# Performance work log

Hardware: AMD Instinct MI355X
Metric: run time of the kernel (lower is better)

## Reference

```python
import jax, jax.numpy as jnp
import numpy as np

N, IN, OUT, K = 4096, 512, 256, 3
ALPHA, BETA, ETA = 0.2, 0.1, 0.5
NEG_INF = -9e15


def setup_inputs() -> dict:
    key = jax.random.key(0)
    k1, k2, k3, k4, k5, k6 = jax.random.split(key, 6)
    h = jax.random.normal(k1, (N, IN), dtype=jnp.float32)
    # xavier-ish scale for params
    W = jax.random.normal(k2, (K * IN, OUT), dtype=jnp.float32) * (1.414 / np.sqrt(IN + OUT))
    a = jax.random.normal(k3, (2 * OUT * K, 1), dtype=jnp.float32) * 0.05
    disc = jax.random.normal(k4, (2 * OUT, 1), dtype=jnp.float32) * 0.05
    k_mask = jax.random.randint(k5, (K, N, N), 0, 2).astype(jnp.int32)  # 0/1 k-hop masks
    lamda = jax.random.uniform(k6, (1,), dtype=jnp.float32)
    return {"h": h, "W": W, "a": a, "disc": disc, "k_mask": k_mask, "lamda": lamda}


def reference(h, W, a, disc, k_mask, lamda):
    lam = lamda[0]
    Wk = W.reshape(K, IN, OUT)          # W[i*IN:(i+1)*IN] per hop
    ak = a.reshape(K, 2, OUT)           # a[2*hop*OUT:(2*hop+2)*OUT] per hop, split in two
    d = disc.reshape(2, OUT)

    # Per-hop projections. In the torch loop Wh is recomputed from h each hop,
    # so only hop 0 determines the returned features; all hops feed dischange.
    Wh_all = jnp.einsum('ni,kio->kno', h, Wk)  # [K, N, OUT]

    # dischange = sum_i eta^i * (Wh_i @ d1 + (Wh_i @ d2).T)  -- rank-1 separable
    wts = ETA ** jnp.arange(K, dtype=jnp.float32)            # [K]
    dv1 = jnp.einsum('kno,o->kn', Wh_all, d[0])              # [K, N]
    dv2 = jnp.einsum('kno,o->kn', Wh_all, d[1])
    u = jnp.einsum('k,kn->n', wts, dv1)
    v = jnp.einsum('k,kn->n', wts, dv2)
    dischange = u[:, None] + v[None, :]                      # [N, N]

    # hop-0 masked GAT attention
    Wh0 = Wh_all[0]
    s1 = Wh0 @ ak[0, 0]                                      # [N]
    s2 = Wh0 @ ak[0, 1]
    e = jax.nn.leaky_relu(s1[:, None] + s2[None, :], ALPHA)  # [N, N]
    att = jax.nn.softmax(jnp.where(k_mask[0] > 0, e, NEG_INF), axis=1)
    # dropout disabled (eval mode / training=False)
    Wh = (1.0 - BETA) * (att @ Wh0) + BETA * Wh0
    out = jax.nn.elu(Wh)

    # normalize dischange and threshold against lamda
    dn = dischange / jnp.maximum(jnp.abs(dischange.min()), dischange.max())
    pos = (dn > lam).astype(jnp.int32)
    dn = jnp.where(dn > lam, 0.0, dn)
    neg = (dn < -lam).astype(jnp.int32)
    dn = jnp.where(dn < -lam, 0.0, dn)

    # mask lists computed from ORIGINAL masks, then applied sequentially
    pos_list = [((k_mask[i] + pos) >= 2).astype(jnp.int32) for i in range(K - 1)]
    neg_list = [((k_mask[i] + neg) >= 2).astype(jnp.int32) for i in range(1, K)]
    km = k_mask
    for i in range(1, K):
        km = km.at[i].add(pos_list[i - 1])
        km = km.at[i - 1].add(-pos_list[i - 1])
    for i in range(K - 1):
        km = km.at[i + 1].add(neg_list[i])
        km = km.at[i].add(-neg_list[i])

    return out, dn, km
```

## Files before the change

### kernel.cpp

```cpp
#include <hip/hip_runtime.h>
#include <hip/hip_bf16.h>
#include <math.h>

#define N 4096
#define DIN 512
#define DOUT 256
#define JS 8
#define JCH (N / JS)

typedef short bf16x8 __attribute__((ext_vector_type(8)));
typedef float f32x4 __attribute__((ext_vector_type(4)));
typedef int i32x4 __attribute__((ext_vector_type(4)));

static __device__ __forceinline__ unsigned short f2bf(float x) {
  __hip_bfloat16 b = __float2bfloat16(x);
  return __builtin_bit_cast(unsigned short, b);
}

static __device__ __forceinline__ unsigned int f2ord(float f) {
  unsigned int b = __float_as_uint(f);
  return (b & 0x80000000u) ? ~b : (b | 0x80000000u);
}
static __device__ __forceinline__ float ord2f(unsigned int u) {
  unsigned int b = (u & 0x80000000u) ? (u ^ 0x80000000u) : ~u;
  return __uint_as_float(b);
}

__global__ __launch_bounds__(256) void k_pq(const float* __restrict__ W,
                                            const float* __restrict__ disc,
                                            double* __restrict__ p, double* __restrict__ q,
                                            unsigned int* __restrict__ smaxw) {
  if (blockIdx.x == 0 && threadIdx.x == 0) smaxw[0] = 0u;
  __shared__ double lds[8];
  int i = blockIdx.x;
  int t = threadIdx.x;
  double accp = 0.0, accq = 0.0;
  const double wts[3] = {1.0, 0.5, 0.25};
#pragma unroll
  for (int k = 0; k < 3; ++k) {
    double w = (double)W[((size_t)(k * DIN + i)) * DOUT + t];
    accp += wts[k] * w * (double)disc[t];
    accq += wts[k] * w * (double)disc[DOUT + t];
  }
  for (int off = 32; off; off >>= 1) { accp += __shfl_down(accp, off); accq += __shfl_down(accq, off); }
  int l = t & 63, w_ = t >> 6;
  if (l == 0) { lds[w_] = accp; lds[4 + w_] = accq; }
  __syncthreads();
  if (t == 0) {
    p[i] = lds[0] + lds[1] + lds[2] + lds[3];
    q[i] = lds[4] + lds[5] + lds[6] + lds[7];
  }
}

__global__ __launch_bounds__(256) void k_uv(const float* __restrict__ h,
                                            const double* __restrict__ p, const double* __restrict__ q,
                                            double* __restrict__ u, double* __restrict__ v) {
  __shared__ double lds[8];
  int n = blockIdx.x, t = threadIdx.x;
  double su = 0.0, sv = 0.0;
#pragma unroll
  for (int i = t; i < DIN; i += 256) {
    double hv = (double)h[(size_t)n * DIN + i];
    su += hv * p[i];
    sv += hv * q[i];
  }
  for (int off = 32; off; off >>= 1) { su += __shfl_down(su, off); sv += __shfl_down(sv, off); }
  int l = t & 63, w_ = t >> 6;
  if (l == 0) { lds[w_] = su; lds[4 + w_] = sv; }
  __syncthreads();
  if (t == 0) {
    u[n] = lds[0] + lds[1] + lds[2] + lds[3];
    v[n] = lds[4] + lds[5] + lds[6] + lds[7];
  }
}

__global__ __launch_bounds__(1024) void k_denom(const double* __restrict__ u,
                                                const double* __restrict__ v,
                                                double* __restrict__ scal) {
  __shared__ double lds[64];
  int t = threadIdx.x;
  double mnu = 1e300, mxu = -1e300, mnv = 1e300, mxv = -1e300;
#pragma unroll
  for (int k = 0; k < 4; ++k) {
    double uu = u[t + k * 1024], vv = v[t + k * 1024];
    mnu = fmin(mnu, uu); mxu = fmax(mxu, uu);
    mnv = fmin(mnv, vv); mxv = fmax(mxv, vv);
  }
  for (int off = 32; off; off >>= 1) {
    mnu = fmin(mnu, __shfl_down(mnu, off)); mxu = fmax(mxu, __shfl_down(mxu, off));
    mnv = fmin(mnv, __shfl_down(mnv, off)); mxv = fmax(mxv, __shfl_down(mxv, off));
  }
  int l = t & 63, w_ = t >> 6;
  if (l == 0) { lds[w_] = mnu; lds[16 + w_] = mxu; lds[32 + w_] = mnv; lds[48 + w_] = mxv; }
  __syncthreads();
  if (t == 0) {
    double a = 1e300, b = -1e300, c = 1e300, d = -1e300;
    for (int k = 0; k < 16; ++k) {
      a = fmin(a, lds[k]); b = fmax(b, lds[16 + k]);
      c = fmin(c, lds[32 + k]); d = fmax(d, lds[48 + k]);
    }
    double mn = a + c, mx = b + d;
    scal[0] = 1.0 / fmax(fabs(mn), mx);
  }
}

__global__ __launch_bounds__(256) void k_dnkm(const int* __restrict__ kmask,
                                              const double* __restrict__ u, const double* __restrict__ v,
                                              const double* __restrict__ scal, const float* __restrict__ lamda,
                                              float* __restrict__ dn, float* __restrict__ kmout) {
  const size_t NN = (size_t)N * N;
  const int* k0 = kmask; const int* k1 = kmask + NN; const int* k2 = kmask + 2 * NN;
  float* km0 = kmout; float* km1 = kmout + NN; float* km2 = kmout + 2 * NN;
  const size_t total4 = NN / 4;
  double inv = scal[0];
  double lam = (double)lamda[0];
  for (size_t idx = (size_t)blockIdx.x * 256 + threadIdx.x; idx < total4;
       idx += (size_t)gridDim.x * 256) {
    int i = (int)(idx >> 10);
    int j = (int)(idx & 1023) << 2;
    size_t base = (size_t)i * N + j;
    double ui = u[i];
    double2 va = *(const double2*)(v + j);
    double2 vb = *(const double2*)(v + j + 2);
    double vv[4] = {va.x, va.y, vb.x, vb.y};
    i32x4 m0 = __builtin_nontemporal_load((const i32x4*)(k0 + base));
    i32x4 m1 = __builtin_nontemporal_load((const i32x4*)(k1 + base));
    i32x4 m2 = __builtin_nontemporal_load((const i32x4*)(k2 + base));
    f32x4 odn, o0, o1, o2;
#pragma unroll
    for (int c = 0; c < 4; ++c) {
      double dnv = (ui + vv[c]) * inv;
      bool pos = dnv > lam, neg = dnv < -lam;
      float dnf = (pos || neg) ? 0.0f : (float)dnv;
      int mk0 = m0[c], mk1 = m1[c], mk2 = m2[c];
      int p0 = pos ? mk0 : 0;
      int p1 = pos ? mk1 : 0;
      int n0 = neg ? mk1 : 0;
      int n1 = neg ? mk2 : 0;
      odn[c] = dnf;
      o0[c] = (float)(mk0 - p0 - n0);
      o1[c] = (float)(mk1 + p0 - p1 + n0 - n1);
      o2[c] = (float)(mk2 + p1 + n1);
    }
    __builtin_nontemporal_store(odn, (f32x4*)(dn + base));
    __builtin_nontemporal_store(o0, (f32x4*)(km0 + base));
    __builtin_nontemporal_store(o1, (f32x4*)(km1 + base));
    __builtin_nontemporal_store(o2, (f32x4*)(km2 + base));
  }
}

__global__ __launch_bounds__(256) void k_wh0(const float* __restrict__ h, const float* __restrict__ W,
                                             float* __restrict__ Wh0, unsigned short* __restrict__ Wh0T) {
  __shared__ float As[32][20];
  __shared__ float Bs[16][72];
  int t = threadIdx.x;
  int i0 = blockIdx.x * 32, o0 = blockIdx.y * 64;
  int tx = t & 15, ty = t >> 4;
  float acc[2][4] = {};
  int am = t >> 2, ak = (t & 3) * 4;
  int bk = t >> 4, bn = (t & 15) * 4;
  float4 pa, pb;
  if (t < 128) pa = *(const float4*)(h + (size_t)(i0 + am) * DIN + ak);
  pb = *(const float4*)(W + (size_t)bk * DOUT + o0 + bn);
  for (int kb = 0; kb < DIN; kb += 16) {
    if (t < 128) *(float4*)&As[am][ak] = pa;
    *(float4*)&Bs[bk][bn] = pb;
    __syncthreads();
    if (kb + 16 < DIN) {
      if (t < 128) pa = *(const float4*)(h + (size_t)(i0 + am) * DIN + kb + 16 + ak);
      pb = *(const float4*)(W + (size_t)(kb + 16 + bk) * DOUT + o0 + bn);
    }
#pragma unroll
    for (int kk = 0; kk < 16; ++kk) {
      float a0 = As[ty * 2 + 0][kk], a1 = As[ty * 2 + 1][kk];
      float4 b = *(const float4*)&Bs[kk][tx * 4];
      acc[0][0] += a0 * b.x; acc[0][1] += a0 * b.y; acc[0][2] += a0 * b.z; acc[0][3] += a0 * b.w;
      acc[1][0] += a1 * b.x; acc[1][1] += a1 * b.y; acc[1][2] += a1 * b.z; acc[1][3] += a1 * b.w;
    }
    __syncthreads();
  }
#pragma unroll
  for (int r = 0; r < 2; ++r) {
    int n = i0 + ty * 2 + r;
    float4 vo = {acc[r][0], acc[r][1], acc[r][2], acc[r][3]};
    *(float4*)(Wh0 + (size_t)n * DOUT + o0 + tx * 4) = vo;
#pragma unroll
    for (int c = 0; c < 4; ++c) {
      Wh0T[(size_t)(o0 + tx * 4 + c) * N + n] = f2bf(acc[r][c]);
    }
  }
}

__global__ __launch_bounds__(256) void k_s1s2(const float* __restrict__ Wh0, const float* __restrict__ a,
                                              float* __restrict__ s1, float* __restrict__ s2,
                                              unsigned int* __restrict__ smaxw) {
  __shared__ float lds[8];
  int i = blockIdx.x, t = threadIdx.x;
  float val = Wh0[(size_t)i * DOUT + t];
  float v1 = val * a[t];
  float v2 = val * a[DOUT + t];
  for (int off = 32; off; off >>= 1) { v1 += __shfl_down(v1, off); v2 += __shfl_down(v2, off); }
  int l = t & 63, w_ = t >> 6;
  if (l == 0) { lds[w_] = v1; lds[4 + w_] = v2; }
  __syncthreads();
  if (t == 0) {
    s1[i] = lds[0] + lds[1] + lds[2] + lds[3];
    float s2i = lds[4] + lds[5] + lds[6] + lds[7];
    s2[i] = s2i;
    atomicMax(smaxw, f2ord(s2i));
  }
}

__global__ __launch_bounds__(512) void k_attn2(const int* __restrict__ k0,
                                               const float* __restrict__ s1, const float* __restrict__ s2,
                                               const unsigned int* __restrict__ smaxw,
                                               const unsigned short* __restrict__ Wh0T,
                                               float* __restrict__ Opart, float* __restrict__ Zpart) {
  int t = threadIdx.x;
  int w = t >> 6, l = t & 63;
  int o0 = (w & 3) * 64;
  int rbase = blockIdx.x * 32 + (w >> 2) * 16;
  int row = l & 15;
  int kg = l >> 4;
  int irow = rbase + row;
  float s1r = s1[irow];
  float sm2 = ord2f(smaxw[0]);
  float mb = s1r + sm2;
  float mi = mb >= 0.0f ? mb : 0.2f * mb;
  f32x4 acc0 = {0,0,0,0}, acc1 = {0,0,0,0}, acc2 = {0,0,0,0}, acc3 = {0,0,0,0};
  float zacc = 0.0f;
  const unsigned short* bbase = Wh0T + ((size_t)(o0 + row) * N + 8 * kg);
  const int* mbase = k0 + (size_t)irow * N + 8 * kg;
  const float* sbase = s2 + 8 * kg;
  int jbeg = blockIdx.y * JCH;
  for (int j0 = jbeg; j0 < jbeg + JCH; j0 += 32) {
    int4 ma = *(const int4*)(mbase + j0);
    int4 mb4 = *(const int4*)(mbase + j0 + 4);
    float4 sa = *(const float4*)(sbase + j0);
    float4 sb = *(const float4*)(sbase + j0 + 4);
    float pv[8];
#pragma unroll
    for (int c = 0; c < 4; ++c) {
      float sv = s1r + (&sa.x)[c];
      float e = sv >= 0.0f ? sv : 0.2f * sv;
      pv[c] = (&ma.x)[c] > 0 ? __expf(e - mi) : 0.0f;
    }
#pragma unroll
    for (int c = 0; c < 4; ++c) {
      float sv = s1r + (&sb.x)[c];
      float e = sv >= 0.0f ? sv : 0.2f * sv;
      pv[4 + c] = (&mb4.x)[c] > 0 ? __expf(e - mi) : 0.0f;
    }
    bf16x8 af;
#pragma unroll
    for (int c = 0; c < 8; ++c) af[c] = (short)f2bf(pv[c]);
    zacc += pv[0] + pv[1] + pv[2] + pv[3] + pv[4] + pv[5] + pv[6] + pv[7];
    bf16x8 b0 = *(const bf16x8*)(bbase + j0);
    bf16x8 b1 = *(const bf16x8*)(bbase + 16 * N + j0);
    bf16x8 b2 = *(const bf16x8*)(bbase + 32 * N + j0);
    bf16x8 b3 = *(const bf16x8*)(bbase + 48 * N + j0);
    acc0 = __builtin_amdgcn_mfma_f32_16x16x32_bf16(af, b0, acc0, 0, 0, 0);
    acc1 = __builtin_amdgcn_mfma_f32_16x16x32_bf16(af, b1, acc1, 0, 0, 0);
    acc2 = __builtin_amdgcn_mfma_f32_16x16x32_bf16(af, b2, acc2, 0, 0, 0);
    acc3 = __builtin_amdgcn_mfma_f32_16x16x32_bf16(af, b3, acc3, 0, 0, 0);
  }
  zacc += __shfl_xor(zacc, 16);
  zacc += __shfl_xor(zacc, 32);
  if ((w & 3) == 0 && l < 16) Zpart[(size_t)blockIdx.y * N + rbase + l] = zacc;
  float* op = Opart + (size_t)blockIdx.y * N * DOUT;
  int col = l & 15, rw = (l >> 4) * 4;
  f32x4 accs[4] = {acc0, acc1, acc2, acc3};
#pragma unroll
  for (int reg = 0; reg < 4; ++reg) {
    int i = rbase + rw + reg;
#pragma unroll
    for (int os = 0; os < 4; ++os) {
      op[(size_t)i * DOUT + o0 + os * 16 + col] = accs[os][reg];
    }
  }
}

__global__ __launch_bounds__(256) void k_ored(const float* __restrict__ Opart,
                                              const float* __restrict__ Zpart,
                                              const float* __restrict__ Wh0,
                                              float* __restrict__ out) {
  int i = blockIdx.x, t = threadIdx.x;
  size_t idx = (size_t)i * DOUT + t;
  float s = 0.0f, z = 0.0f;
#pragma unroll
  for (int sp = 0; sp < JS; ++sp) {
    s += Opart[(size_t)sp * N * DOUT + idx];
    z += Zpart[(size_t)sp * N + i];
  }
  float val = 0.9f * (s / z) + 0.1f * Wh0[idx];
  out[idx] = val > 0.0f ? val : expm1f(val);
}

extern "C" void kernel_launch(void* const* d_in, const int* in_sizes, int n_in,
                              void* d_out, int out_size, void* d_ws, size_t ws_size,
                              hipStream_t stream) {
  const float* h     = (const float*)d_in[0];
  const float* W     = (const float*)d_in[1];
  const float* a     = (const float*)d_in[2];
  const float* disc  = (const float*)d_in[3];
  const int*   kmask = (const int*)d_in[4];
  const float* lamda = (const float*)d_in[5];

  float* out = (float*)d_out;
  float* dn  = out + (size_t)N * DOUT;
  float* km  = dn + (size_t)N * N;

  char* ws = (char*)d_ws;
  double* p    = (double*)ws;
  double* q    = (double*)(ws + 4096);
  double* u    = (double*)(ws + 8192);
  double* v    = (double*)(ws + 8192 + 32768);
  double* scal = (double*)(ws + 8192 + 65536);
  char* ws2 = ws + 8192 + 65536 + 256;
  float* s1            = (float*)ws2;
  float* s2            = (float*)(ws2 + 16384);
  unsigned int* smaxw  = (unsigned int*)(ws2 + 32768);
  float* Zpart         = (float*)(ws2 + 33024);
  char* ws3 = ws2 + 33024 + (size_t)JS * N * 4;
  float* Wh0           = (float*)ws3;
  unsigned short* Wh0T = (unsigned short*)(ws3 + (size_t)N * DOUT * 4);
  float* Opart         = (float*)(ws3 + (size_t)N * DOUT * 6);

  k_pq<<<DIN, 256, 0, stream>>>(W, disc, p, q, smaxw);
  k_uv<<<N, 256, 0, stream>>>(h, p, q, u, v);
  k_denom<<<1, 1024, 0, stream>>>(u, v, scal);
  k_dnkm<<<4096, 256, 0, stream>>>(kmask, u, v, scal, lamda, dn, km);
  k_wh0<<<dim3(N / 32, DOUT / 64), 256, 0, stream>>>(h, W, Wh0, Wh0T);
  k_s1s2<<<N, 256, 0, stream>>>(Wh0, a, s1, s2, smaxw);
  k_attn2<<<dim3(N / 32, JS), 512, 0, stream>>>(kmask, s1, s2, smaxw, Wh0T, Opart, Zpart);
  k_ored<<<N, 256, 0, stream>>>(Opart, Zpart, Wh0, out);
}
```

Before: 603.5 us.

## Fuse attention-probability computation into k-mask streaming pass and s1/s2 into GEMM

The masked softmax numerators are now computed inside the pass that already streams k_mask[0] for the dn/km outputs. They are written as a bf16 probability matrix P along with per-row sums Z, so the attention MFMA kernel no longer rereads the int32 mask or recomputes exp. The s1/s2 dot products are folded into the Wh0 GEMM epilogue via atomics, and the max reduction moves into a combined prep kernel. This removes a second full read of the 64 MB mask, at the cost of writing and reading a 32 MB bf16 P matrix.

After: 539.6 us. -10.6%, faster.

```diff
diff --git a/kernel.cpp b/kernel.cpp
--- a/kernel.cpp
+++ b/kernel.cpp
@@ -11,29 +11,22 @@
 typedef short bf16x8 __attribute__((ext_vector_type(8)));
 typedef float f32x4 __attribute__((ext_vector_type(4)));
 typedef int i32x4 __attribute__((ext_vector_type(4)));
+typedef unsigned short u16x4 __attribute__((ext_vector_type(4)));
 
 static __device__ __forceinline__ unsigned short f2bf(float x) {
   __hip_bfloat16 b = __float2bfloat16(x);
   return __builtin_bit_cast(unsigned short, b);
 }
 
-static __device__ __forceinline__ unsigned int f2ord(float f) {
-  unsigned int b = __float_as_uint(f);
-  return (b & 0x80000000u) ? ~b : (b | 0x80000000u);
-}
-static __device__ __forceinline__ float ord2f(unsigned int u) {
-  unsigned int b = (u & 0x80000000u) ? (u ^ 0x80000000u) : ~u;
-  return __uint_as_float(b);
-}
-
 __global__ __launch_bounds__(256) void k_pq(const float* __restrict__ W,
                                             const float* __restrict__ disc,
                                             double* __restrict__ p, double* __restrict__ q,
-                                            unsigned int* __restrict__ smaxw) {
-  if (blockIdx.x == 0 && threadIdx.x == 0) smaxw[0] = 0u;
-  __shared__ double lds[8];
+                                            float* __restrict__ s1, float* __restrict__ s2) {
   int i = blockIdx.x;
   int t = threadIdx.x;
+  if (i < 16) s1[i * 256 + t] = 0.0f;
+  else if (i < 32) s2[(i - 16) * 256 + t] = 0.0f;
+  __shared__ double lds[8];
   double accp = 0.0, accq = 0.0;
   const double wts[3] = {1.0, 0.5, 0.25};
 #pragma unroll
@@ -74,83 +67,10 @@
   }
 }
 
-__global__ __launch_bounds__(1024) void k_denom(const double* __restrict__ u,
-                                                const double* __restrict__ v,
-                                                double* __restrict__ scal) {
-  __shared__ double lds[64];
-  int t = threadIdx.x;
-  double mnu = 1e300, mxu = -1e300, mnv = 1e300, mxv = -1e300;
-#pragma unroll
-  for (int k = 0; k < 4; ++k) {
-    double uu = u[t + k * 1024], vv = v[t + k * 1024];
-    mnu = fmin(mnu, uu); mxu = fmax(mxu, uu);
-    mnv = fmin(mnv, vv); mxv = fmax(mxv, vv);
-  }
-  for (int off = 32; off; off >>= 1) {
-    mnu = fmin(mnu, __shfl_down(mnu, off)); mxu = fmax(mxu, __shfl_down(mxu, off));
-    mnv = fmin(mnv, __shfl_down(mnv, off)); mxv = fmax(mxv, __shfl_down(mxv, off));
-  }
-  int l = t & 63, w_ = t >> 6;
-  if (l == 0) { lds[w_] = mnu; lds[16 + w_] = mxu; lds[32 + w_] = mnv; lds[48 + w_] = mxv; }
-  __syncthreads();
-  if (t == 0) {
-    double a = 1e300, b = -1e300, c = 1e300, d = -1e300;
-    for (int k = 0; k < 16; ++k) {
-      a = fmin(a, lds[k]); b = fmax(b, lds[16 + k]);
-      c = fmin(c, lds[32 + k]); d = fmax(d, lds[48 + k]);
-    }
-    double mn = a + c, mx = b + d;
-    scal[0] = 1.0 / fmax(fabs(mn), mx);
-  }
-}
-
-__global__ __launch_bounds__(256) void k_dnkm(const int* __restrict__ kmask,
-                                              const double* __restrict__ u, const double* __restrict__ v,
-                                              const double* __restrict__ scal, const float* __restrict__ lamda,
-                                              float* __restrict__ dn, float* __restrict__ kmout) {
-  const size_t NN = (size_t)N * N;
-  const int* k0 = kmask; const int* k1 = kmask + NN; const int* k2 = kmask + 2 * NN;
-  float* km0 = kmout; float* km1 = kmout + NN; float* km2 = kmout + 2 * NN;
-  const size_t total4 = NN / 4;
-  double inv = scal[0];
-  double lam = (double)lamda[0];
-  for (size_t idx = (size_t)blockIdx.x * 256 + threadIdx.x; idx < total4;
-       idx += (size_t)gridDim.x * 256) {
-    int i = (int)(idx >> 10);
-    int j = (int)(idx & 1023) << 2;
-    size_t base = (size_t)i * N + j;
-    double ui = u[i];
-    double2 va = *(const double2*)(v + j);
-    double2 vb = *(const double2*)(v + j + 2);
-    double vv[4] = {va.x, va.y, vb.x, vb.y};
-    i32x4 m0 = __builtin_nontemporal_load((const i32x4*)(k0 + base));
-    i32x4 m1 = __builtin_nontemporal_load((const i32x4*)(k1 + base));
-    i32x4 m2 = __builtin_nontemporal_load((const i32x4*)(k2 + base));
-    f32x4 odn, o0, o1, o2;
-#pragma unroll
-    for (int c = 0; c < 4; ++c) {
-      double dnv = (ui + vv[c]) * inv;
-      bool pos = dnv > lam, neg = dnv < -lam;
-      float dnf = (pos || neg) ? 0.0f : (float)dnv;
-      int mk0 = m0[c], mk1 = m1[c], mk2 = m2[c];
-      int p0 = pos ? mk0 : 0;
-      int p1 = pos ? mk1 : 0;
-      int n0 = neg ? mk1 : 0;
-      int n1 = neg ? mk2 : 0;
-      odn[c] = dnf;
-      o0[c] = (float)(mk0 - p0 - n0);
-      o1[c] = (float)(mk1 + p0 - p1 + n0 - n1);
-      o2[c] = (float)(mk2 + p1 + n1);
-    }
-    __builtin_nontemporal_store(odn, (f32x4*)(dn + base));
-    __builtin_nontemporal_store(o0, (f32x4*)(km0 + base));
-    __builtin_nontemporal_store(o1, (f32x4*)(km1 + base));
-    __builtin_nontemporal_store(o2, (f32x4*)(km2 + base));
-  }
-}
-
 __global__ __launch_bounds__(256) void k_wh0(const float* __restrict__ h, const float* __restrict__ W,
-                                             float* __restrict__ Wh0, unsigned short* __restrict__ Wh0T) {
+                                             const float* __restrict__ a,
+                                             float* __restrict__ Wh0, unsigned short* __restrict__ Wh0T,
+                                             float* __restrict__ s1, float* __restrict__ s2) {
   __shared__ float As[32][20];
   __shared__ float Bs[16][72];
   int t = threadIdx.x;
@@ -179,6 +99,8 @@
     }
     __syncthreads();
   }
+  float4 a1v = *(const float4*)(a + o0 + tx * 4);
+  float4 a2v = *(const float4*)(a + DOUT + o0 + tx * 4);
 #pragma unroll
   for (int r = 0; r < 2; ++r) {
     int n = i0 + ty * 2 + r;
@@ -188,34 +110,119 @@
     for (int c = 0; c < 4; ++c) {
       Wh0T[(size_t)(o0 + tx * 4 + c) * N + n] = f2bf(acc[r][c]);
     }
-  }
-}
-
-__global__ __launch_bounds__(256) void k_s1s2(const float* __restrict__ Wh0, const float* __restrict__ a,
-                                              float* __restrict__ s1, float* __restrict__ s2,
-                                              unsigned int* __restrict__ smaxw) {
-  __shared__ float lds[8];
-  int i = blockIdx.x, t = threadIdx.x;
-  float val = Wh0[(size_t)i * DOUT + t];
-  float v1 = val * a[t];
-  float v2 = val * a[DOUT + t];
-  for (int off = 32; off; off >>= 1) { v1 += __shfl_down(v1, off); v2 += __shfl_down(v2, off); }
+    float p1 = acc[r][0] * a1v.x + acc[r][1] * a1v.y + acc[r][2] * a1v.z + acc[r][3] * a1v.w;
+    float p2 = acc[r][0] * a2v.x + acc[r][1] * a2v.y + acc[r][2] * a2v.z + acc[r][3] * a2v.w;
+    for (int off = 1; off < 16; off <<= 1) { p1 += __shfl_xor(p1, off); p2 += __shfl_xor(p2, off); }
+    if (tx == 0) { atomicAdd(s1 + n, p1); atomicAdd(s2 + n, p2); }
+  }
+}
+
+__global__ __launch_bounds__(1024) void k_prep(const double* __restrict__ u,
+                                               const double* __restrict__ v,
+                                               const float* __restrict__ s2,
+                                               double* __restrict__ scal,
+                                               float* __restrict__ smaxf) {
+  __shared__ double lds[64];
+  __shared__ float lf[16];
+  int t = threadIdx.x;
+  double mnu = 1e300, mxu = -1e300, mnv = 1e300, mxv = -1e300;
+#pragma unroll
+  for (int k = 0; k < 4; ++k) {
+    double uu = u[t + k * 1024], vv = v[t + k * 1024];
+    mnu = fmin(mnu, uu); mxu = fmax(mxu, uu);
+    mnv = fmin(mnv, vv); mxv = fmax(mxv, vv);
+  }
+  float4 sv = *(const float4*)(s2 + t * 4);
+  float sm = fmaxf(fmaxf(sv.x, sv.y), fmaxf(sv.z, sv.w));
+  for (int off = 32; off; off >>= 1) {
+    mnu = fmin(mnu, __shfl_down(mnu, off)); mxu = fmax(mxu, __shfl_down(mxu, off));
+    mnv = fmin(mnv, __shfl_down(mnv, off)); mxv = fmax(mxv, __shfl_down(mxv, off));
+    sm = fmaxf(sm, __shfl_down(sm, off));
+  }
   int l = t & 63, w_ = t >> 6;
-  if (l == 0) { lds[w_] = v1; lds[4 + w_] = v2; }
+  if (l == 0) { lds[w_] = mnu; lds[16 + w_] = mxu; lds[32 + w_] = mnv; lds[48 + w_] = mxv; lf[w_] = sm; }
   __syncthreads();
   if (t == 0) {
-    s1[i] = lds[0] + lds[1] + lds[2] + lds[3];
-    float s2i = lds[4] + lds[5] + lds[6] + lds[7];
-    s2[i] = s2i;
-    atomicMax(smaxw, f2ord(s2i));
-  }
-}
-
-__global__ __launch_bounds__(512) void k_attn2(const int* __restrict__ k0,
-                                               const float* __restrict__ s1, const float* __restrict__ s2,
-                                               const unsigned int* __restrict__ smaxw,
+    double a = 1e300, b = -1e300, c = 1e300, d = -1e300;
+    float s = -1e30f;
+    for (int k = 0; k < 16; ++k) {
+      a = fmin(a, lds[k]); b = fmax(b, lds[16 + k]);
+      c = fmin(c, lds[32 + k]); d = fmax(d, lds[48 + k]);
+      s = fmaxf(s, lf[k]);
+    }
+    scal[0] = 1.0 / fmax(fabs(a + c), b + d);
+    smaxf[0] = s;
+  }
+}
+
+__global__ __launch_bounds__(256) void k_dnkm(const int* __restrict__ kmask,
+                                              const double* __restrict__ u, const double* __restrict__ v,
+                                              const double* __restrict__ scal, const float* __restrict__ lamda,
+                                              const float* __restrict__ s1, const float* __restrict__ s2,
+                                              const float* __restrict__ smaxf,
+                                              float* __restrict__ dn, float* __restrict__ kmout,
+                                              unsigned short* __restrict__ P, float* __restrict__ Z) {
+  const size_t NN = (size_t)N * N;
+  const int* k0 = kmask; const int* k1 = kmask + NN; const int* k2 = kmask + 2 * NN;
+  float* km0 = kmout; float* km1 = kmout + NN; float* km2 = kmout + 2 * NN;
+  int r = blockIdx.x, t = threadIdx.x;
+  double inv = scal[0];
+  double lam = (double)lamda[0];
+  double ui = u[r];
+  float s1r = s1[r];
+  float mb = s1r + smaxf[0];
+  float mi = mb >= 0.0f ? mb : 0.2f * mb;
+  float zacc = 0.0f;
+#pragma unroll
+  for (int k = 0; k < 4; ++k) {
+    int j = k * 1024 + t * 4;
+    size_t base = (size_t)r * N + j;
+    double2 va = *(const double2*)(v + j);
+    double2 vb = *(const double2*)(v + j + 2);
+    double vv[4] = {va.x, va.y, vb.x, vb.y};
+    i32x4 m0 = __builtin_nontemporal_load((const i32x4*)(k0 + base));
+    i32x4 m1 = __builtin_nontemporal_load((const i32x4*)(k1 + base));
+    i32x4 m2 = __builtin_nontemporal_load((const i32x4*)(k2 + base));
+    float4 sv = *(const float4*)(s2 + j);
+    f32x4 odn, o0, o1, o2;
+    u16x4 pw;
+#pragma unroll
+    for (int c = 0; c < 4; ++c) {
+      double dnv = (ui + vv[c]) * inv;
+      bool pos = dnv > lam, neg = dnv < -lam;
+      float dnf = (pos || neg) ? 0.0f : (float)dnv;
+      int mk0 = m0[c], mk1 = m1[c], mk2 = m2[c];
+      int p0 = pos ? mk0 : 0;
+      int p1 = pos ? mk1 : 0;
+      int n0 = neg ? mk1 : 0;
+      int n1 = neg ? mk2 : 0;
+      odn[c] = dnf;
+      o0[c] = (float)(mk0 - p0 - n0);
+      o1[c] = (float)(mk1 + p0 - p1 + n0 - n1);
+      o2[c] = (float)(mk2 + p1 + n1);
+      float e = s1r + (&sv.x)[c];
+      e = e >= 0.0f ? e : 0.2f * e;
+      float pv = mk0 > 0 ? __expf(e - mi) : 0.0f;
+      pw[c] = f2bf(pv);
+      zacc += pv;
+    }
+    __builtin_nontemporal_store(odn, (f32x4*)(dn + base));
+    __builtin_nontemporal_store(o0, (f32x4*)(km0 + base));
+    __builtin_nontemporal_store(o1, (f32x4*)(km1 + base));
+    __builtin_nontemporal_store(o2, (f32x4*)(km2 + base));
+    *(u16x4*)(P + base) = pw;
+  }
+  __shared__ float lf[4];
+  for (int off = 32; off; off >>= 1) zacc += __shfl_down(zacc, off);
+  int l = t & 63, w_ = t >> 6;
+  if (l == 0) lf[w_] = zacc;
+  __syncthreads();
+  if (t == 0) Z[r] = lf[0] + lf[1] + lf[2] + lf[3];
+}
+
+__global__ __launch_bounds__(512) void k_attn2(const unsigned short* __restrict__ P,
                                                const unsigned short* __restrict__ Wh0T,
-                                               float* __restrict__ Opart, float* __restrict__ Zpart) {
+                                               float* __restrict__ Opart) {
   int t = threadIdx.x;
   int w = t >> 6, l = t & 63;
   int o0 = (w & 3) * 64;
@@ -223,38 +230,13 @@
   int row = l & 15;
   int kg = l >> 4;
   int irow = rbase + row;
-  float s1r = s1[irow];
-  float sm2 = ord2f(smaxw[0]);
-  float mb = s1r + sm2;
-  float mi = mb >= 0.0f ? mb : 0.2f * mb;
   f32x4 acc0 = {0,0,0,0}, acc1 = {0,0,0,0}, acc2 = {0,0,0,0}, acc3 = {0,0,0,0};
-  float zacc = 0.0f;
+  const unsigned short* abase = P + (size_t)irow * N + 8 * kg;
   const unsigned short* bbase = Wh0T + ((size_t)(o0 + row) * N + 8 * kg);
-  const int* mbase = k0 + (size_t)irow * N + 8 * kg;
-  const float* sbase = s2 + 8 * kg;
   int jbeg = blockIdx.y * JCH;
+#pragma unroll 4
   for (int j0 = jbeg; j0 < jbeg + JCH; j0 += 32) {
-    int4 ma = *(const int4*)(mbase + j0);
-    int4 mb4 = *(const int4*)(mbase + j0 + 4);
-    float4 sa = *(const float4*)(sbase + j0);
-    float4 sb = *(const float4*)(sbase + j0 + 4);
-    float pv[8];
-#pragma unroll
-    for (int c = 0; c < 4; ++c) {
-      float sv = s1r + (&sa.x)[c];
-      float e = sv >= 0.0f ? sv : 0.2f * sv;
-      pv[c] = (&ma.x)[c] > 0 ? __expf(e - mi) : 0.0f;
-    }
-#pragma unroll
-    for (int c = 0; c < 4; ++c) {
-      float sv = s1r + (&sb.x)[c];
-      float e = sv >= 0.0f ? sv : 0.2f * sv;
-      pv[4 + c] = (&mb4.x)[c] > 0 ? __expf(e - mi) : 0.0f;
-    }
-    bf16x8 af;
-#pragma unroll
-    for (int c = 0; c < 8; ++c) af[c] = (short)f2bf(pv[c]);
-    zacc += pv[0] + pv[1] + pv[2] + pv[3] + pv[4] + pv[5] + pv[6] + pv[7];
+    bf16x8 af = *(const bf16x8*)(abase + j0);
     bf16x8 b0 = *(const bf16x8*)(bbase + j0);
     bf16x8 b1 = *(const bf16x8*)(bbase + 16 * N + j0);
     bf16x8 b2 = *(const bf16x8*)(bbase + 32 * N + j0);
@@ -264,9 +246,6 @@
     acc2 = __builtin_amdgcn_mfma_f32_16x16x32_bf16(af, b2, acc2, 0, 0, 0);
     acc3 = __builtin_amdgcn_mfma_f32_16x16x32_bf16(af, b3, acc3, 0, 0, 0);
   }
-  zacc += __shfl_xor(zacc, 16);
-  zacc += __shfl_xor(zacc, 32);
-  if ((w & 3) == 0 && l < 16) Zpart[(size_t)blockIdx.y * N + rbase + l] = zacc;
   float* op = Opart + (size_t)blockIdx.y * N * DOUT;
   int col = l & 15, rw = (l >> 4) * 4;
   f32x4 accs[4] = {acc0, acc1, acc2, acc3};
@@ -281,18 +260,15 @@
 }
 
 __global__ __launch_bounds__(256) void k_ored(const float* __restrict__ Opart,
-                                              const float* __restrict__ Zpart,
+                                              const float* __restrict__ Z,
                                               const float* __restrict__ Wh0,
                                               float* __restrict__ out) {
   int i = blockIdx.x, t = threadIdx.x;
   size_t idx = (size_t)i * DOUT + t;
-  float s = 0.0f, z = 0.0f;
-#pragma unroll
-  for (int sp = 0; sp < JS; ++sp) {
-    s += Opart[(size_t)sp * N * DOUT + idx];
-    z += Zpart[(size_t)sp * N + i];
-  }
-  float val = 0.9f * (s / z) + 0.1f * Wh0[idx];
+  float s = 0.0f;
+#pragma unroll
+  for (int sp = 0; sp < JS; ++sp) s += Opart[(size_t)sp * N * DOUT + idx];
+  float val = 0.9f * (s / Z[i]) + 0.1f * Wh0[idx];
   out[idx] = val > 0.0f ? val : expm1f(val);
 }
 
@@ -316,22 +292,22 @@
   double* u    = (double*)(ws + 8192);
   double* v    = (double*)(ws + 8192 + 32768);
   double* scal = (double*)(ws + 8192 + 65536);
+  float* smaxf = (float*)(ws + 8192 + 65536 + 64);
   char* ws2 = ws + 8192 + 65536 + 256;
-  float* s1            = (float*)ws2;
-  float* s2            = (float*)(ws2 + 16384);
-  unsigned int* smaxw  = (unsigned int*)(ws2 + 32768);
-  float* Zpart         = (float*)(ws2 + 33024);
-  char* ws3 = ws2 + 33024 + (size_t)JS * N * 4;
+  float* s1 = (float*)ws2;
+  float* s2 = (float*)(ws2 + 16384);
+  float* Z  = (float*)(ws2 + 32768);
+  char* ws3 = ws2 + 49152;
   float* Wh0           = (float*)ws3;
   unsigned short* Wh0T = (unsigned short*)(ws3 + (size_t)N * DOUT * 4);
-  float* Opart         = (float*)(ws3 + (size_t)N * DOUT * 6);
-
-  k_pq<<<DIN, 256, 0, stream>>>(W, disc, p, q, smaxw);
+  unsigned short* P    = (unsigned short*)(ws3 + (size_t)N * DOUT * 6);
+  float* Opart         = (float*)(ws3 + (size_t)N * DOUT * 6 + (size_t)N * N * 2);
+
+  k_pq<<<DIN, 256, 0, stream>>>(W, disc, p, q, s1, s2);
   k_uv<<<N, 256, 0, stream>>>(h, p, q, u, v);
-  k_denom<<<1, 1024, 0, stream>>>(u, v, scal);
-  k_dnkm<<<4096, 256, 0, stream>>>(kmask, u, v, scal, lamda, dn, km);
-  k_wh0<<<dim3(N / 32, DOUT / 64), 256, 0, stream>>>(h, W, Wh0, Wh0T);
-  k_s1s2<<<N, 256, 0, stream>>>(Wh0, a, s1, s2, smaxw);
-  k_attn2<<<dim3(N / 32, JS), 512, 0, stream>>>(kmask, s1, s2, smaxw, Wh0T, Opart, Zpart);
-  k_ored<<<N, 256, 0, stream>>>(Opart, Zpart, Wh0, out);
-}
+  k_wh0<<<dim3(N / 32, DOUT / 64), 256, 0, stream>>>(h, W, a, Wh0, Wh0T, s1, s2);
+  k_prep<<<1, 1024, 0, stream>>>(u, v, s2, scal, smaxf);
+  k_dnkm<<<N, 256, 0, stream>>>(kmask, u, v, scal, lamda, s1, s2, smaxf, dn, km, P, Z);
+  k_attn2<<<dim3(N / 32, JS), 512, 0, stream>>>(P, Wh0T, Opart);
+  k_ored<<<N, 256, 0, stream>>>(Opart, Z, Wh0, out);
+}
```
